# Kernel optimization log

Measured on AMD Instinct MI355X. Metric: run time of the kernel, lower is better.

The kernel has to match this reference:

```python
import jax, jax.numpy as jnp
import numpy as np

N = 50000
E = 800000
G_DIM = 128
H1 = 128
H2 = 32
HEADS = 4
R = 8            # 2 * n_speakers**2, n_speakers=2
NUM_BASES = 20
NEG_SLOPE = 0.2  # PyG GATConv default


def setup_inputs() -> dict:
    key = jax.random.key(0)
    ks = jax.random.split(key, 12)
    node_features = jax.random.normal(ks[0], (N, G_DIM), dtype=jnp.float32)
    edge_index = jax.random.randint(ks[1], (2, E), 0, N, dtype=jnp.int64)
    edge_type = jax.random.randint(ks[2], (E,), 0, R, dtype=jnp.int64)
    s = 0.1
    comp = jax.random.normal(ks[3], (R, NUM_BASES), dtype=jnp.float32) * s
    basis = jax.random.normal(ks[4], (NUM_BASES, G_DIM, H1), dtype=jnp.float32) * s
    root = jax.random.normal(ks[5], (G_DIM, H1), dtype=jnp.float32) * s
    bias1 = jax.random.normal(ks[6], (H1,), dtype=jnp.float32) * s
    gat_w = jax.random.normal(ks[7], (H1, HEADS * H2), dtype=jnp.float32) * s
    att_src = jax.random.normal(ks[8], (HEADS, H2), dtype=jnp.float32) * s
    att_dst = jax.random.normal(ks[9], (HEADS, H2), dtype=jnp.float32) * s
    gat_bias = jax.random.normal(ks[10], (HEADS * H2,), dtype=jnp.float32) * s
    return {
        "node_features": node_features,
        "edge_index": edge_index,
        "edge_type": edge_type,
        "comp": comp,
        "basis": basis,
        "root": root,
        "bias1": bias1,
        "gat_w": gat_w,
        "att_src": att_src,
        "att_dst": att_dst,
        "gat_bias": gat_bias,
    }


def _rgcn(x, src, dst, edge_type, comp, basis, root, bias):
    # Basis-decomposed relation weights: [R, G_DIM, H1]
    W = jnp.einsum('rb,bio->rio', comp, basis)
    xj = x[src]  # [E, G_DIM] gather (memory-bound)
    out0 = jnp.zeros((N, W.shape[2]), dtype=x.dtype)

    def step(out, wr):
        Wr, r = wr
        mask = (edge_type == r).astype(x.dtype)  # [E]
        ssum = jax.ops.segment_sum(xj * mask[:, None], dst, num_segments=N)  # [N, G_DIM]
        cnt = jax.ops.segment_sum(mask, dst, num_segments=N)                 # [N]
        mean = jnp.where(cnt[:, None] > 0, ssum / jnp.maximum(cnt, 1.0)[:, None], 0.0)
        return out + mean @ Wr, None

    out, _ = jax.lax.scan(step, out0, (W, jnp.arange(R)))
    return out + x @ root + bias  # PyG RGCNConv root weight + bias


def _gat(x, src, dst, gat_w, att_src, att_dst, gat_bias):
    xl = (x @ gat_w).reshape(N, HEADS, H2)           # [N, H, D]
    a_src = jnp.einsum('nhd,hd->nh', xl, att_src)    # [N, H]
    a_dst = jnp.einsum('nhd,hd->nh', xl, att_dst)
    # PyG default: remove existing self-loops, then add one self-loop per node.
    loop = jnp.arange(N)
    s2 = jnp.concatenate([src, loop])
    d2 = jnp.concatenate([dst, loop])
    valid = jnp.concatenate([src != dst, jnp.ones((N,), dtype=bool)])
    alpha = jax.nn.leaky_relu(a_src[s2] + a_dst[d2], NEG_SLOPE)  # [E+N, H]
    alpha = jnp.where(valid[:, None], alpha, -jnp.inf)
    # segment softmax over incoming edges per destination node
    m = jax.ops.segment_max(alpha, d2, num_segments=N)           # [N, H]
    ea = jnp.exp(alpha - m[d2])
    denom = jax.ops.segment_sum(ea, d2, num_segments=N)          # [N, H]
    alpha = ea / denom[d2]
    msg = xl[s2] * alpha[:, :, None]                             # [E+N, H, D]
    out = jax.ops.segment_sum(msg, d2, num_segments=N)           # [N, H, D]
    return out.reshape(N, HEADS * H2) + gat_bias                 # concat heads + bias


def reference(node_features, edge_index, edge_type, comp, basis, root, bias1,
              gat_w, att_src, att_dst, gat_bias):
    src, dst = edge_index[0], edge_index[1]
    h = _rgcn(node_features, src, dst, edge_type, comp, basis, root, bias1)
    return _gat(h, src, dst, gat_w, att_src, att_dst, gat_bias)
```

## Files before the change

kernel.cpp:

```cpp
#include <hip/hip_runtime.h>
#include <hip/hip_bf16.h>

#define RREL 8
#define NB 20
#define KEXT 1152
#define CAP 16

typedef __attribute__((ext_vector_type(8))) short bf16x8;
typedef __attribute__((ext_vector_type(4))) float f32x4;

static inline int cdiv(long a, long b){ return (int)((a + b - 1)/b); }

__device__ inline float2 b2f2(unsigned u){
  union { unsigned u; __hip_bfloat162 b; } c; c.u = u;
  return __bfloat1622float2(c.b);
}
__device__ inline unsigned f2b2(float x, float y){
  float2 f; f.x = x; f.y = y;
  union { unsigned u; __hip_bfloat162 b; } c; c.b = __float22bfloat162_rn(f);
  return c.u;
}

__device__ inline long wpack_idx(int k, int o){
  int ks = k >> 5, nt = o >> 4;
  int lane = (((k >> 3) & 3) << 4) | (o & 15);
  return ((long)((ks*8 + nt)*64 + lane))*8 + (k & 7);
}

__device__ inline int cnt_of(unsigned long long u0, unsigned long long u1, int r){
  unsigned long long u = (r < 4) ? u0 : u1;
  int c = (int)((u >> ((r & 3)*16)) & 0xFFFFull);
  return (c < CAP) ? c : CAP;
}

__global__ __launch_bounds__(256) void k_prep(const float* __restrict__ comp,
    const float* __restrict__ basis, const float* __restrict__ root,
    const float* __restrict__ gatw, const float* __restrict__ x,
    __hip_bfloat16* __restrict__ Wb, __hip_bfloat16* __restrict__ Wg,
    __hip_bfloat16* __restrict__ xb, int Nn)
{
  int bid = blockIdx.x, t = threadIdx.x;
  if (bid < 576) {
    int idx = bid*256 + t;
    int k = idx >> 7, o = idx & 127;
    float s;
    if (k < 1024) {
      int r = k >> 7, io = ((k & 127) << 7) | o;
      s = 0.f;
      #pragma unroll
      for (int b = 0; b < NB; ++b) s += comp[r*NB + b] * basis[b*16384 + io];
    } else {
      s = root[((k - 1024) << 7) | o];
    }
    Wb[wpack_idx(k, o)] = __float2bfloat16(s);
  } else if (bid < 640) {
    int idx = (bid - 576)*256 + t;
    int k = idx >> 7, o = idx & 127;
    Wg[wpack_idx(k, o)] = __float2bfloat16(gatw[idx]);
  } else {
    int i = (bid - 640)*256 + t;
    if (i >= Nn*16) return;
    const float4* ip = (const float4*)x;
    float4 f0 = ip[i*2], f1 = ip[i*2+1];
    uint4 o4;
    o4.x = f2b2(f0.x, f0.y); o4.y = f2b2(f0.z, f0.w);
    o4.z = f2b2(f1.x, f1.y); o4.w = f2b2(f1.z, f1.w);
    ((uint4*)xb)[i] = o4;
  }
}

__global__ __launch_bounds__(256) void k_permute(const int* __restrict__ src,
    const int* __restrict__ dst, const int* __restrict__ et,
    int* __restrict__ cnt16, unsigned short* __restrict__ packed16, int E, int Nn)
{
  int e = blockIdx.x*256 + threadIdx.x;
  if (e >= E) return;
  int d = dst[e], s = src[e], r = et[e];
  int p = atomicAdd(&cnt16[d*8 + r], 1);
  p = (p < CAP) ? p : (CAP - 1);
  packed16[((long)r*Nn + d)*CAP + p] = (unsigned short)s;
}

#define NPB 16
__global__ __launch_bounds__(256) void k_rgcn(const unsigned short* __restrict__ packed16,
    const int* __restrict__ cnt16,
    const __hip_bfloat16* __restrict__ xb, const __hip_bfloat16* __restrict__ Wb,
    const __hip_bfloat16* __restrict__ Wg, const float* __restrict__ bias1,
    const float* __restrict__ attS, const float* __restrict__ attD,
    __hip_bfloat16* __restrict__ xlb, float* __restrict__ aS,
    float* __restrict__ aD, int Nn)
{
  __shared__ short S[NPB*KEXT + 16*128];
  int t = threadIdx.x, lane = t & 63, wv = t >> 6;
  int qt = lane >> 4, ql = lane & 15;
  int n0 = blockIdx.x * NPB;
  char* Sbase = (char*)S;
  char* hLbase = (char*)S + NPB*KEXT*2;

  for (int i = t; i < NPB*KEXT/8; i += 256) ((uint4*)S)[i] = make_uint4(0,0,0,0);
  __syncthreads();

  int nl = wv*4 + qt;
  int n = n0 + nl;
  char* Sr = Sbase + (long)nl*(KEXT*2);
  unsigned swz = (unsigned)((nl & 7) << 4);
  int dg = 0;
  unsigned long long u0 = 0, u1 = 0;
  if (n < Nn) {
    *(uint4*)(Sr + ((2048u + ql*16) ^ swz)) =
        *(const uint4*)&xb[(long)n*128 + ql*8];
    int4 ca = *(const int4*)&cnt16[n*8];
    int4 cb = *(const int4*)&cnt16[n*8 + 4];
    u0 = (unsigned long long)(unsigned)ca.x | ((unsigned long long)(unsigned)ca.y << 16)
       | ((unsigned long long)(unsigned)ca.z << 32) | ((unsigned long long)(unsigned)ca.w << 48);
    u1 = (unsigned long long)(unsigned)cb.x | ((unsigned long long)(unsigned)cb.y << 16)
       | ((unsigned long long)(unsigned)cb.z << 32) | ((unsigned long long)(unsigned)cb.w << 48);
    #pragma unroll
    for (int r = 0; r < 8; ++r) dg += cnt_of(u0, u1, r);
  }
  float a[8] = {};
  int prA = 0, startA = 0, endA = cnt_of(u0, u1, 0);
  int prB = 0, endB = endA;
  for (int e0 = 0; e0 < dg; e0 += 8) {
    int addr[8]; unsigned short srcs[8]; uint4 vv[8];
    #pragma unroll
    for (int j = 0; j < 8; ++j) {
      int ii = e0 + j; ii = (ii < dg) ? ii : (dg - 1);
      while (ii >= endA) { prA++; startA = endA; endA += cnt_of(u0, u1, prA); }
      addr[j] = (prA*Nn + n)*CAP + (ii - startA);
    }
    #pragma unroll
    for (int j = 0; j < 8; ++j) srcs[j] = packed16[addr[j]];
    #pragma unroll
    for (int j = 0; j < 8; ++j)
      vv[j] = *(const uint4*)&xb[(long)srcs[j]*128 + ql*8];
    #pragma unroll
    for (int j = 0; j < 8; ++j) {
      int idx = e0 + j;
      if (idx < dg) {
        while (idx >= endB) {
          int c = cnt_of(u0, u1, prB);
          if (c > 0) {
            float sc = __builtin_amdgcn_rcpf((float)c);
            uint4 w4;
            w4.x = f2b2(a[0]*sc, a[1]*sc); w4.y = f2b2(a[2]*sc, a[3]*sc);
            w4.z = f2b2(a[4]*sc, a[5]*sc); w4.w = f2b2(a[6]*sc, a[7]*sc);
            *(uint4*)(Sr + (((unsigned)(prB*256 + ql*16)) ^ swz)) = w4;
            #pragma unroll
            for (int cc = 0; cc < 8; ++cc) a[cc] = 0.f;
          }
          prB++; endB += cnt_of(u0, u1, prB);
        }
        float2 v0 = b2f2(vv[j].x), v1 = b2f2(vv[j].y);
        float2 v2 = b2f2(vv[j].z), v3 = b2f2(vv[j].w);
        a[0] += v0.x; a[1] += v0.y; a[2] += v1.x; a[3] += v1.y;
        a[4] += v2.x; a[5] += v2.y; a[6] += v3.x; a[7] += v3.y;
      }
    }
  }
  if (dg > 0) {
    int c = cnt_of(u0, u1, prB);
    if (c > 0) {
      float sc = __builtin_amdgcn_rcpf((float)c);
      uint4 w4;
      w4.x = f2b2(a[0]*sc, a[1]*sc); w4.y = f2b2(a[2]*sc, a[3]*sc);
      w4.z = f2b2(a[4]*sc, a[5]*sc); w4.w = f2b2(a[6]*sc, a[7]*sc);
      *(uint4*)(Sr + (((unsigned)(prB*256 + ql*16)) ^ swz)) = w4;
    }
  }
  __syncthreads();

  int col = lane & 15, q = lane >> 4;
  int nt0 = wv*2, nt1 = nt0 + 1;
  const bf16x8* W8 = (const bf16x8*)Wb;
  f32x4 c0 = {0.f,0.f,0.f,0.f}, c1 = {0.f,0.f,0.f,0.f};
  unsigned rswz = (unsigned)((col & 7) << 4);
  for (int ks = 0; ks < KEXT/32; ++ks) {
    bf16x8 av = *(const bf16x8*)(Sbase + (long)col*(KEXT*2)
                                 + (((unsigned)(ks*64 + q*16)) ^ rswz));
    bf16x8 b0 = W8[(ks*8 + nt0)*64 + lane];
    bf16x8 b1 = W8[(ks*8 + nt1)*64 + lane];
    c0 = __builtin_amdgcn_mfma_f32_16x16x32_bf16(av, b0, c0, 0, 0, 0);
    c1 = __builtin_amdgcn_mfma_f32_16x16x32_bf16(av, b1, c1, 0, 0, 0);
  }
  #pragma unroll
  for (int r = 0; r < 4; ++r) {
    int row = q*4 + r;
    unsigned hswz = (unsigned)((row & 7) << 4);
    *(short*)(hLbase + (((unsigned)(row*256 + (nt0*16 + col)*2)) ^ hswz)) =
        (short)__bfloat16_as_ushort(__float2bfloat16(c0[r] + bias1[nt0*16 + col]));
    *(short*)(hLbase + (((unsigned)(row*256 + (nt1*16 + col)*2)) ^ hswz)) =
        (short)__bfloat16_as_ushort(__float2bfloat16(c1[r] + bias1[nt1*16 + col]));
  }
  __syncthreads();

  const bf16x8* Wg8 = (const bf16x8*)Wg;
  f32x4 d0 = {0.f,0.f,0.f,0.f}, d1 = {0.f,0.f,0.f,0.f};
  #pragma unroll
  for (int ks = 0; ks < 4; ++ks) {
    bf16x8 av = *(const bf16x8*)(hLbase + (((unsigned)(col*256 + ks*64 + q*16)) ^ rswz));
    bf16x8 b0 = Wg8[(ks*8 + nt0)*64 + lane];
    bf16x8 b1 = Wg8[(ks*8 + nt1)*64 + lane];
    d0 = __builtin_amdgcn_mfma_f32_16x16x32_bf16(av, b0, d0, 0, 0, 0);
    d1 = __builtin_amdgcn_mfma_f32_16x16x32_bf16(av, b1, d1, 0, 0, 0);
  }
  #pragma unroll
  for (int r = 0; r < 4; ++r) {
    int row = n0 + q*4 + r;
    if (row < Nn) {
      xlb[(long)row*128 + nt0*16 + col] = __float2bfloat16(d0[r]);
      xlb[(long)row*128 + nt1*16 + col] = __float2bfloat16(d1[r]);
    }
  }
  float s0 = attS[wv*32 + col], s1 = attS[wv*32 + 16 + col];
  float dd0 = attD[wv*32 + col], dd1 = attD[wv*32 + 16 + col];
  #pragma unroll
  for (int r = 0; r < 4; ++r) {
    float sA = d0[r]*s0 + d1[r]*s1;
    float sD = d0[r]*dd0 + d1[r]*dd1;
    #pragma unroll
    for (int d = 1; d < 16; d <<= 1) {
      sA += __shfl_xor(sA, d);
      sD += __shfl_xor(sD, d);
    }
    int row = n0 + q*4 + r;
    if (col == 0 && row < Nn) {
      aS[(long)row*4 + wv] = sA;
      aD[(long)row*4 + wv] = sD;
    }
  }
}

__device__ inline float lrelu(float v){ return v > 0.f ? v : 0.2f*v; }

__global__ __launch_bounds__(256) void k_gat(const unsigned short* __restrict__ packed16,
    const int* __restrict__ cnt16,
    const float* __restrict__ aS, const float* __restrict__ aD,
    const __hip_bfloat16* __restrict__ xlb, const float* __restrict__ gatb,
    float* __restrict__ out, int Nn)
{
  int lane = threadIdx.x & 63;
  int wvg = (blockIdx.x*256 + threadIdx.x) >> 6;
  int qt = lane >> 4, ql = lane & 15;
  int n = wvg*4 + qt;
  int hh = ql >> 2;
  bool act = (n < Nn);
  int dg = 0;
  unsigned long long u0 = 0, u1 = 0;
  float aSn = 0.f, aDn = 0.f;
  uint4 xs = make_uint4(0,0,0,0);
  if (act) {
    int4 ca = *(const int4*)&cnt16[n*8];
    int4 cb = *(const int4*)&cnt16[n*8 + 4];
    u0 = (unsigned long long)(unsigned)ca.x | ((unsigned long long)(unsigned)ca.y << 16)
       | ((unsigned long long)(unsigned)ca.z << 32) | ((unsigned long long)(unsigned)ca.w << 48);
    u1 = (unsigned long long)(unsigned)cb.x | ((unsigned long long)(unsigned)cb.y << 16)
       | ((unsigned long long)(unsigned)cb.z << 32) | ((unsigned long long)(unsigned)cb.w << 48);
    #pragma unroll
    for (int r = 0; r < 8; ++r) dg += cnt_of(u0, u1, r);
    aSn = aS[(long)n*4 + hh]; aDn = aD[(long)n*4 + hh];
    xs = *(const uint4*)&xlb[(long)n*128 + ql*8];
  }
  float wself = __expf(lrelu(aSn + aDn));
  float den = wself;
  float2 x0 = b2f2(xs.x), x1 = b2f2(xs.y), x2 = b2f2(xs.z), x3 = b2f2(xs.w);
  float acc[8] = {x0.x*wself, x0.y*wself, x1.x*wself, x1.y*wself,
                  x2.x*wself, x2.y*wself, x3.x*wself, x3.y*wself};

  int prA = 0, startA = 0, endA = cnt_of(u0, u1, 0);
  for (int e0 = 0; e0 < dg; e0 += 8) {
    int addr[8]; unsigned short srcs[8]; uint4 vv[8]; float as_[8];
    #pragma unroll
    for (int j = 0; j < 8; ++j) {
      int ii = e0 + j; ii = (ii < dg) ? ii : (dg - 1);
      while (ii >= endA) { prA++; startA = endA; endA += cnt_of(u0, u1, prA); }
      addr[j] = (prA*Nn + n)*CAP + (ii - startA);
    }
    #pragma unroll
    for (int j = 0; j < 8; ++j) srcs[j] = packed16[addr[j]];
    #pragma unroll
    for (int j = 0; j < 8; ++j) {
      as_[j] = aS[(long)srcs[j]*4 + hh];
      vv[j]  = *(const uint4*)&xlb[(long)srcs[j]*128 + ql*8];
    }
    #pragma unroll
    for (int j = 0; j < 8; ++j) {
      bool ok = (e0 + j < dg) && (srcs[j] != (unsigned short)n);
      float w = __expf(lrelu(as_[j] + aDn));
      w = ok ? w : 0.f;
      den += w;
      float2 v0 = b2f2(vv[j].x), v1 = b2f2(vv[j].y);
      float2 v2 = b2f2(vv[j].z), v3 = b2f2(vv[j].w);
      acc[0] = fmaf(v0.x, w, acc[0]); acc[1] = fmaf(v0.y, w, acc[1]);
      acc[2] = fmaf(v1.x, w, acc[2]); acc[3] = fmaf(v1.y, w, acc[3]);
      acc[4] = fmaf(v2.x, w, acc[4]); acc[5] = fmaf(v2.y, w, acc[5]);
      acc[6] = fmaf(v3.x, w, acc[6]); acc[7] = fmaf(v3.y, w, acc[7]);
    }
  }
  if (act) {
    float rd = 1.f / den;
    float4 g0 = *(const float4*)&gatb[ql*8];
    float4 g1 = *(const float4*)&gatb[ql*8 + 4];
    float4 r0, r1;
    r0.x = acc[0]*rd + g0.x; r0.y = acc[1]*rd + g0.y;
    r0.z = acc[2]*rd + g0.z; r0.w = acc[3]*rd + g0.w;
    r1.x = acc[4]*rd + g1.x; r1.y = acc[5]*rd + g1.y;
    r1.z = acc[6]*rd + g1.z; r1.w = acc[7]*rd + g1.w;
    *(float4*)&out[(long)n*128 + ql*8]     = r0;
    *(float4*)&out[(long)n*128 + ql*8 + 4] = r1;
  }
}

extern "C" void kernel_launch(void* const* d_in, const int* in_sizes, int n_in,
                              void* d_out, int out_size, void* d_ws, size_t ws_size,
                              hipStream_t stream) {
  const float* x     = (const float*)d_in[0];
  const int*   eidx  = (const int*)  d_in[1];
  const int*   etype = (const int*)  d_in[2];
  const float* comp  = (const float*)d_in[3];
  const float* basis = (const float*)d_in[4];
  const float* root  = (const float*)d_in[5];
  const float* bias1 = (const float*)d_in[6];
  const float* gatw  = (const float*)d_in[7];
  const float* attS  = (const float*)d_in[8];
  const float* attD  = (const float*)d_in[9];
  const float* gatb  = (const float*)d_in[10];

  int Nn = in_sizes[0] / 128;
  int E  = in_sizes[2];
  const int* src = eidx;
  const int* dst = eidx + E;

  char* ws = (char*)d_ws;
  size_t o = 0;
  auto alloc = [&](size_t bytes) { void* p = ws + o; o = (o + bytes + 255) & ~(size_t)255; return p; };
  __hip_bfloat16* Wb  = (__hip_bfloat16*)alloc((size_t)KEXT*128*2);
  __hip_bfloat16* Wg  = (__hip_bfloat16*)alloc((size_t)128*128*2);
  __hip_bfloat16* xb  = (__hip_bfloat16*)alloc((size_t)Nn*128*2);
  __hip_bfloat16* xlb = (__hip_bfloat16*)alloc((size_t)Nn*128*2);
  float* aS   = (float*)alloc((size_t)Nn*4*4);
  float* aD   = (float*)alloc((size_t)Nn*4*4);
  int*   cnt16 = (int*)alloc((size_t)Nn*RREL*4);
  unsigned short* packed16 = (unsigned short*)alloc((size_t)RREL*Nn*CAP*2);

  float* out = (float*)d_out;

  hipMemsetAsync(cnt16, 0, (size_t)Nn*RREL*4, stream);

  int cvtB = cdiv((long)Nn*16, 256);
  k_prep<<<640 + cvtB, 256, 0, stream>>>(comp, basis, root, gatw, x, Wb, Wg, xb, Nn);
  k_permute<<<cdiv(E,256), 256, 0, stream>>>(src, dst, etype, cnt16, packed16, E, Nn);

  k_rgcn<<<cdiv(Nn,NPB), 256, 0, stream>>>(packed16, cnt16, xb, Wb, Wg, bias1,
                                           attS, attD, xlb, aS, aD, Nn);
  k_gat<<<cdiv((long)Nn*16,256), 256, 0, stream>>>(packed16, cnt16, aS, aD, xlb, gatb, out, Nn);
}
```

Before: 176.0 us.

## Merge edge bucketing into prep kernel and store buckets node-major

The separate k_permute launch is folded into k_prep as extra blocks, which removes one kernel launch and lets the edge bucketing run alongside the weight and feature conversion. The packed source-index buffer changes from relation-major to node-major ([node][rel][CAP]), so each node's edge lists sit in one contiguous 256-byte region. This should make the index reads in k_rgcn and k_gat more local. The cost is that atomic-driven scattered writes now share a kernel with the conversion work.

After: 185.1 us. +5.2%, slower.

```diff
diff --git a/kernel.cpp b/kernel.cpp
--- a/kernel.cpp
+++ b/kernel.cpp
@@ -36,10 +36,14 @@
 __global__ __launch_bounds__(256) void k_prep(const float* __restrict__ comp,
     const float* __restrict__ basis, const float* __restrict__ root,
     const float* __restrict__ gatw, const float* __restrict__ x,
+    const int* __restrict__ src, const int* __restrict__ dst,
+    const int* __restrict__ et,
     __hip_bfloat16* __restrict__ Wb, __hip_bfloat16* __restrict__ Wg,
-    __hip_bfloat16* __restrict__ xb, int Nn)
+    __hip_bfloat16* __restrict__ xb, int* __restrict__ cnt16,
+    unsigned short* __restrict__ packed16, int Nn, int E)
 {
   int bid = blockIdx.x, t = threadIdx.x;
+  int cvtB = (Nn*16 + 255) >> 8;
   if (bid < 576) {
     int idx = bid*256 + t;
     int k = idx >> 7, o = idx & 127;
@@ -57,7 +61,7 @@
     int idx = (bid - 576)*256 + t;
     int k = idx >> 7, o = idx & 127;
     Wg[wpack_idx(k, o)] = __float2bfloat16(gatw[idx]);
-  } else {
+  } else if (bid < 640 + cvtB) {
     int i = (bid - 640)*256 + t;
     if (i >= Nn*16) return;
     const float4* ip = (const float4*)x;
@@ -66,19 +70,14 @@
     o4.x = f2b2(f0.x, f0.y); o4.y = f2b2(f0.z, f0.w);
     o4.z = f2b2(f1.x, f1.y); o4.w = f2b2(f1.z, f1.w);
     ((uint4*)xb)[i] = o4;
-  }
-}
-
-__global__ __launch_bounds__(256) void k_permute(const int* __restrict__ src,
-    const int* __restrict__ dst, const int* __restrict__ et,
-    int* __restrict__ cnt16, unsigned short* __restrict__ packed16, int E, int Nn)
-{
-  int e = blockIdx.x*256 + threadIdx.x;
-  if (e >= E) return;
-  int d = dst[e], s = src[e], r = et[e];
-  int p = atomicAdd(&cnt16[d*8 + r], 1);
-  p = (p < CAP) ? p : (CAP - 1);
-  packed16[((long)r*Nn + d)*CAP + p] = (unsigned short)s;
+  } else {
+    int e = (bid - 640 - cvtB)*256 + t;
+    if (e >= E) return;
+    int d = dst[e], s = src[e], r = et[e];
+    int p = atomicAdd(&cnt16[d*8 + r], 1);
+    p = (p < CAP) ? p : (CAP - 1);
+    packed16[((long)d*8 + r)*CAP + p] = (unsigned short)s;
+  }
 }
 
 #define NPB 16
@@ -106,6 +105,7 @@
   unsigned swz = (unsigned)((nl & 7) << 4);
   int dg = 0;
   unsigned long long u0 = 0, u1 = 0;
+  long bbase = (long)n*8*CAP;
   if (n < Nn) {
     *(uint4*)(Sr + ((2048u + ql*16) ^ swz)) =
         *(const uint4*)&xb[(long)n*128 + ql*8];
@@ -122,12 +122,12 @@
   int prA = 0, startA = 0, endA = cnt_of(u0, u1, 0);
   int prB = 0, endB = endA;
   for (int e0 = 0; e0 < dg; e0 += 8) {
-    int addr[8]; unsigned short srcs[8]; uint4 vv[8];
+    long addr[8]; unsigned short srcs[8]; uint4 vv[8];
     #pragma unroll
     for (int j = 0; j < 8; ++j) {
       int ii = e0 + j; ii = (ii < dg) ? ii : (dg - 1);
       while (ii >= endA) { prA++; startA = endA; endA += cnt_of(u0, u1, prA); }
-      addr[j] = (prA*Nn + n)*CAP + (ii - startA);
+      addr[j] = bbase + prA*CAP + (ii - startA);
     }
     #pragma unroll
     for (int j = 0; j < 8; ++j) srcs[j] = packed16[addr[j]];
@@ -249,6 +249,7 @@
   unsigned long long u0 = 0, u1 = 0;
   float aSn = 0.f, aDn = 0.f;
   uint4 xs = make_uint4(0,0,0,0);
+  long bbase = (long)n*8*CAP;
   if (act) {
     int4 ca = *(const int4*)&cnt16[n*8];
     int4 cb = *(const int4*)&cnt16[n*8 + 4];
@@ -269,12 +270,12 @@
 
   int prA = 0, startA = 0, endA = cnt_of(u0, u1, 0);
   for (int e0 = 0; e0 < dg; e0 += 8) {
-    int addr[8]; unsigned short srcs[8]; uint4 vv[8]; float as_[8];
+    long addr[8]; unsigned short srcs[8]; uint4 vv[8]; float as_[8];
     #pragma unroll
     for (int j = 0; j < 8; ++j) {
       int ii = e0 + j; ii = (ii < dg) ? ii : (dg - 1);
       while (ii >= endA) { prA++; startA = endA; endA += cnt_of(u0, u1, prA); }
-      addr[j] = (prA*Nn + n)*CAP + (ii - startA);
+      addr[j] = bbase + prA*CAP + (ii - startA);
     }
     #pragma unroll
     for (int j = 0; j < 8; ++j) srcs[j] = packed16[addr[j]];
@@ -341,16 +342,17 @@
   float* aS   = (float*)alloc((size_t)Nn*4*4);
   float* aD   = (float*)alloc((size_t)Nn*4*4);
   int*   cnt16 = (int*)alloc((size_t)Nn*RREL*4);
-  unsigned short* packed16 = (unsigned short*)alloc((size_t)RREL*Nn*CAP*2);
+  unsigned short* packed16 = (unsigned short*)alloc((size_t)Nn*RREL*CAP*2);
 
   float* out = (float*)d_out;
 
   hipMemsetAsync(cnt16, 0, (size_t)Nn*RREL*4, stream);
 
   int cvtB = cdiv((long)Nn*16, 256);
-  k_prep<<<640 + cvtB, 256, 0, stream>>>(comp, basis, root, gatw, x, Wb, Wg, xb, Nn);
-  k_permute<<<cdiv(E,256), 256, 0, stream>>>(src, dst, etype, cnt16, packed16, E, Nn);
-
+  int permB = cdiv(E, 256);
+  k_prep<<<640 + cvtB + permB, 256, 0, stream>>>(comp, basis, root, gatw, x,
+                                                 src, dst, etype, Wb, Wg, xb,
+                                                 cnt16, packed16, Nn, E);
   k_rgcn<<<cdiv(Nn,NPB), 256, 0, stream>>>(packed16, cnt16, xb, Wb, Wg, bias1,
                                            attS, attD, xlb, aS, aD, Nn);
   k_gat<<<cdiv((long)Nn*16,256), 256, 0, stream>>>(packed16, cnt16, aS, aD, xlb, gatb, out, Nn);
```
